# Kernel tuning notes

Measured on AMD Instinct MI355X. Metric: run time of the kernel, lower is better.

The kernel has to match this reference:

```python
import jax, jax.numpy as jnp
import numpy as np

EPS = 1e-12

def l2norm(x, axis):
    # torch.nn.functional.normalize: x / max(||x||_2, eps)
    n = jnp.sqrt(jnp.sum(x * x, axis=axis, keepdims=True))
    return x / jnp.maximum(n, EPS)

def setup_inputs() -> dict:
    key = jax.random.key(0)
    k1, k2, k3, k4 = jax.random.split(key, 4)
    B, Cf, H, W = 128, 1024, 16, 16
    n_att, dv = 312, 300
    img = jax.random.normal(k1, (B, Cf, H, W), dtype=jnp.float32)
    # V is initialized from row-normalized w2v embeddings in the module
    V = l2norm(jax.random.normal(k2, (n_att, dv), dtype=jnp.float32), axis=1)
    W1 = jax.random.normal(k3, (dv, Cf), dtype=jnp.float32)
    W2 = jax.random.normal(k4, (dv, Cf), dtype=jnp.float32)
    return {"img": img, "V": V, "W1": W1, "W2": W2}

def reference(img, V, W1, W2):
    vv = l2norm(V, axis=1)                               # [i, v]
    B, Cf, H, Wd = img.shape
    av = l2norm(img.reshape(B, Cf, H * Wd), axis=1)      # [b, f, r]
    Q = vv @ W1                                          # [i, f]
    A = jnp.einsum('if,bfr->bir', Q, av)                 # attention logits
    A = jax.nn.softmax(A, axis=-1)
    F_p = jnp.einsum('bir,bfr->bif', A, av)              # attended features
    Pred_att = jnp.einsum('if,bif->bi', vv @ W2, F_p)
    return Pred_att
```

## Files before the change

kernel.cpp:

```cpp
#include <hip/hip_runtime.h>
#include <math.h>

#define NB   128
#define CF   1024
#define RR   256
#define NA   312
#define DV   300
#define M2   320
#define MT   640
#define NKC  32

typedef _Float16 half8  __attribute__((ext_vector_type(8)));
typedef float float16v  __attribute__((ext_vector_type(16)));
typedef float float4v   __attribute__((ext_vector_type(4)));

__device__ __forceinline__ void gll16(const void* g, void* l) {
    __builtin_amdgcn_global_load_lds(
        (const __attribute__((address_space(1))) void*)g,
        (__attribute__((address_space(3))) void*)l, 16, 0, 0);
}

__global__ void k_pq(const float* __restrict__ img, float* __restrict__ ssq4,
                     _Float16* __restrict__ avT,
                     const float* __restrict__ V, const float* __restrict__ W1,
                     const float* __restrict__ W2, _Float16* __restrict__ Qb) {
    int lin = blockIdx.x;
    if (lin < 512) {
        int q = lin & 3, b = lin >> 2;
        int t = threadIdx.x;
        int kk8 = t & 3;
        int rq  = t >> 2;
        float ss0 = 0.f, ss1 = 0.f, ss2 = 0.f, ss3 = 0.f;
        int kc0 = q * 8;
        for (int kc = kc0; kc < kc0 + 8; ++kc) {
            const float* src = img + ((size_t)b * CF + kc * 32 + kk8 * 8) * RR + rq * 4;
            float4v v[8];
            #pragma unroll
            for (int j = 0; j < 8; ++j) v[j] = *(const float4v*)(src + (size_t)j * RR);
            #pragma unroll
            for (int j = 0; j < 8; ++j) {
                ss0 += v[j][0] * v[j][0]; ss1 += v[j][1] * v[j][1];
                ss2 += v[j][2] * v[j][2]; ss3 += v[j][3] * v[j][3];
            }
            _Float16* dst = avT + ((size_t)(b * NKC + kc) * RR + rq * 4) * 32 + kk8 * 8;
            #pragma unroll
            for (int s = 0; s < 4; ++s) {
                half8 o;
                #pragma unroll
                for (int j = 0; j < 8; ++j) o[j] = (_Float16)v[j][s];
                *(half8*)(dst + (size_t)s * 32) = o;
            }
        }
        ss0 += __shfl_xor(ss0, 1, 64); ss0 += __shfl_xor(ss0, 2, 64);
        ss1 += __shfl_xor(ss1, 1, 64); ss1 += __shfl_xor(ss1, 2, 64);
        ss2 += __shfl_xor(ss2, 1, 64); ss2 += __shfl_xor(ss2, 2, 64);
        ss3 += __shfl_xor(ss3, 1, 64); ss3 += __shfl_xor(ss3, 2, 64);
        if (kk8 == 0) {
            float4v sv; sv[0] = ss0; sv[1] = ss1; sv[2] = ss2; sv[3] = ss3;
            *(float4v*)(ssq4 + ((size_t)b * 4 + q) * RR + rq * 4) = sv;
        }
    } else {
        int m   = lin - 512;
        int ib  = m % 160;
        int fch = m / 160;
        int t   = threadIdx.x;
        int f   = fch * 256 + t;
        bool isQ2 = ib >= 80;
        int i0l = (ib - (isQ2 ? 80 : 0)) * 4;
        int i0g = (isQ2 ? M2 : 0) + i0l;
        __shared__ float inv4[4];
        float acc[4] = {0, 0, 0, 0};
        bool zero = (i0l >= NA);
        if (!zero) {
            int row = t >> 6, l64 = t & 63;
            float s = 0.f;
            for (int v = l64; v < DV; v += 64) { float x = V[(i0l + row) * DV + v]; s += x * x; }
            #pragma unroll
            for (int o = 32; o; o >>= 1) s += __shfl_xor(s, o, 64);
            if (l64 == 0) inv4[row] = 1.f / fmaxf(sqrtf(s), 1e-12f);
            __syncthreads();
            const float* W = isQ2 ? W2 : W1;
            for (int v = 0; v < DV; v += 4) {
                float w0 = W[(size_t)(v + 0) * CF + f];
                float w1 = W[(size_t)(v + 1) * CF + f];
                float w2 = W[(size_t)(v + 2) * CF + f];
                float w3 = W[(size_t)(v + 3) * CF + f];
                #pragma unroll
                for (int ii = 0; ii < 4; ++ii) {
                    const float* Vr = V + (size_t)(i0l + ii) * DV + v;
                    acc[ii] += Vr[0] * w0 + Vr[1] * w1 + Vr[2] * w2 + Vr[3] * w3;
                }
            }
            #pragma unroll
            for (int ii = 0; ii < 4; ++ii) acc[ii] *= inv4[ii];
        }
        #pragma unroll
        for (int ii = 0; ii < 4; ++ii)
            Qb[((size_t)(f >> 5) * MT + (i0g + ii)) * 32 + (f & 31)] = (_Float16)acc[ii];
    }
}

__launch_bounds__(256, 2)
__global__ void k_gemm(const _Float16* __restrict__ Qb, const _Float16* __restrict__ avT,
                       const float* __restrict__ ssq4, float* __restrict__ out) {
    int lin  = blockIdx.x;
    int xcd  = lin & 7;
    int slot = lin >> 3;
    int bq   = slot / 5;
    int t2   = slot - bq * 5;
    int b    = bq * 8 + xcd;

    int tid = threadIdx.x;
    int lane = tid & 63, w = tid >> 6;
    int nl = lane & 31, kh = lane >> 5;

    __shared__ __align__(16) char smem[49152];
    _Float16* A0 = (_Float16*)smem;
    _Float16* A1 = (_Float16*)(smem + 8192);
    _Float16* B0 = (_Float16*)(smem + 16384);
    _Float16* B1 = (_Float16*)(smem + 32768);
    float* mred = (float*)smem;
    float* mg   = (float*)(smem + 1024);
    float* sred = (float*)(smem + 1280);
    float* dred = (float*)(smem + 2304);

    float16v acc[4][2];
    #pragma unroll
    for (int i = 0; i < 4; ++i)
        #pragma unroll
        for (int j = 0; j < 2; ++j)
            #pragma unroll
            for (int gi = 0; gi < 16; ++gi) acc[i][j][gi] = 0.f;

    int arow  = tid & 127;
    int akb0  = tid >> 7;
    int grow  = (arow < 64) ? (t2 * 64 + arow) : (M2 + t2 * 64 + (arow - 64));
    size_t a_src0 = (size_t)grow * 32 + akb0 * 8;
    const _Float16* bpanel = avT + (size_t)b * NKC * RR * 32;

    #define STAGE(kc_, Ab, Bb) do {                                                  \
        const _Float16* as_ = Qb + (size_t)(kc_) * MT * 32 + a_src0;                 \
        gll16(as_,      (char*)(Ab) + tid * 16);                                     \
        gll16(as_ + 16, (char*)(Ab) + tid * 16 + 4096);                              \
        const _Float16* bs_ = bpanel + (size_t)(kc_) * RR * 32 + (size_t)tid * 32;   \
        gll16(bs_,      (char*)(Bb) + tid * 16);                                     \
        gll16(bs_ + 8,  (char*)(Bb) + tid * 16 + 4096);                              \
        gll16(bs_ + 16, (char*)(Bb) + tid * 16 + 8192);                              \
        gll16(bs_ + 24, (char*)(Bb) + tid * 16 + 12288);                             \
    } while (0)

    #define COMPUTE(Al, Bl) do {                                                     \
        _Pragma("unroll")                                                            \
        for (int ks = 0; ks < 2; ++ks) {                                             \
            int kb = ks * 2 + kh;                                                    \
            half8 b0f = *(const half8*)((Bl) + ((size_t)kb * 256 + w * 64 + nl) * 8);       \
            half8 b1f = *(const half8*)((Bl) + ((size_t)kb * 256 + w * 64 + 32 + nl) * 8);  \
            _Pragma("unroll")                                                        \
            for (int rf = 0; rf < 4; ++rf) {                                         \
                half8 af = *(const half8*)((Al) + ((size_t)kb * 128 + rf * 32 + nl) * 8);   \
                acc[rf][0] = __builtin_amdgcn_mfma_f32_32x32x16_f16(af, b0f, acc[rf][0], 0, 0, 0); \
                acc[rf][1] = __builtin_amdgcn_mfma_f32_32x32x16_f16(af, b1f, acc[rf][1], 0, 0, 0); \
            }                                                                        \
        }                                                                            \
    } while (0)

    STAGE(0, A0, B0);
    STAGE(1, A1, B1);
    asm volatile("s_waitcnt vmcnt(6)" ::: "memory");
    __builtin_amdgcn_s_barrier();
    __builtin_amdgcn_sched_barrier(0);

    #pragma unroll 1
    for (int kc = 0; kc < NKC - 2; kc += 2) {
        COMPUTE(A0, B0);
        __builtin_amdgcn_s_barrier();
        __builtin_amdgcn_sched_barrier(0);
        STAGE(kc + 2, A0, B0);
        asm volatile("s_waitcnt vmcnt(6)" ::: "memory");
        __builtin_amdgcn_s_barrier();
        __builtin_amdgcn_sched_barrier(0);
        COMPUTE(A1, B1);
        __builtin_amdgcn_s_barrier();
        __builtin_amdgcn_sched_barrier(0);
        STAGE(kc + 3, A1, B1);
        asm volatile("s_waitcnt vmcnt(6)" ::: "memory");
        __builtin_amdgcn_s_barrier();
        __builtin_amdgcn_sched_barrier(0);
    }
    COMPUTE(A0, B0);
    asm volatile("s_waitcnt vmcnt(0)" ::: "memory");
    __builtin_amdgcn_s_barrier();
    __builtin_amdgcn_sched_barrier(0);
    COMPUTE(A1, B1);

    #undef STAGE
    #undef COMPUTE

    const float* sq = ssq4 + (size_t)b * 4 * RR;
    int c0 = w * 64 + nl;
    float p0 = sq[c0]      + sq[RR + c0]      + sq[2 * RR + c0]      + sq[3 * RR + c0];
    float p1 = sq[32 + c0] + sq[RR + 32 + c0] + sq[2 * RR + 32 + c0] + sq[3 * RR + 32 + c0];
    float iv0 = 1.f / fmaxf(sqrtf(p0), 1e-12f);
    float iv1 = 1.f / fmaxf(sqrtf(p1), 1e-12f);
    #pragma unroll
    for (int rf = 0; rf < 4; ++rf)
        #pragma unroll
        for (int gi = 0; gi < 16; ++gi) {
            acc[rf][0][gi] *= iv0;
            acc[rf][1][gi] *= iv1;
        }

    float mx[2][16];
    #pragma unroll
    for (int p = 0; p < 2; ++p)
        #pragma unroll
        for (int gi = 0; gi < 16; ++gi)
            mx[p][gi] = fmaxf(acc[p][0][gi], acc[p][1][gi]);
    #pragma unroll
    for (int off = 1; off <= 16; off <<= 1)
        #pragma unroll
        for (int p = 0; p < 2; ++p)
            #pragma unroll
            for (int gi = 0; gi < 16; ++gi)
                mx[p][gi] = fmaxf(mx[p][gi], __shfl_xor(mx[p][gi], off, 64));
    if (nl == 0) {
        #pragma unroll
        for (int p = 0; p < 2; ++p)
            #pragma unroll
            for (int gi = 0; gi < 16; ++gi) {
                int row = (gi & 3) + 8 * (gi >> 2) + 4 * kh;
                mred[(p * 32 + row) * 4 + w] = mx[p][gi];
            }
    }
    __syncthreads();
    if (tid < 64)
        mg[tid] = fmaxf(fmaxf(mred[tid * 4], mred[tid * 4 + 1]),
                        fmaxf(mred[tid * 4 + 2], mred[tid * 4 + 3]));
    __syncthreads();
    float sp[2][16], dp[2][16];
    #pragma unroll
    for (int p = 0; p < 2; ++p)
        #pragma unroll
        for (int gi = 0; gi < 16; ++gi) {
            int row = (gi & 3) + 8 * (gi >> 2) + 4 * kh;
            float m  = mg[p * 32 + row];
            float e0 = __expf(acc[p][0][gi] - m);
            float e1 = __expf(acc[p][1][gi] - m);
            sp[p][gi] = e0 + e1;
            dp[p][gi] = e0 * acc[p + 2][0][gi] + e1 * acc[p + 2][1][gi];
        }
    #pragma unroll
    for (int off = 1; off <= 16; off <<= 1)
        #pragma unroll
        for (int p = 0; p < 2; ++p)
            #pragma unroll
            for (int gi = 0; gi < 16; ++gi) {
                sp[p][gi] += __shfl_xor(sp[p][gi], off, 64);
                dp[p][gi] += __shfl_xor(dp[p][gi], off, 64);
            }
    if (nl == 0) {
        #pragma unroll
        for (int p = 0; p < 2; ++p)
            #pragma unroll
            for (int gi = 0; gi < 16; ++gi) {
                int row = (gi & 3) + 8 * (gi >> 2) + 4 * kh;
                sred[(p * 32 + row) * 4 + w] = sp[p][gi];
                dred[(p * 32 + row) * 4 + w] = dp[p][gi];
            }
    }
    __syncthreads();
    if (tid < 64) {
        float s = sred[tid * 4] + sred[tid * 4 + 1] + sred[tid * 4 + 2] + sred[tid * 4 + 3];
        float d = dred[tid * 4] + dred[tid * 4 + 1] + dred[tid * 4 + 2] + dred[tid * 4 + 3];
        int ig = t2 * 64 + tid;
        if (ig < NA) out[b * NA + ig] = d / s;
    }
}

extern "C" void kernel_launch(void* const* d_in, const int* in_sizes, int n_in,
                              void* d_out, int out_size, void* d_ws, size_t ws_size,
                              hipStream_t stream) {
    const float* img = (const float*)d_in[0];
    const float* V   = (const float*)d_in[1];
    const float* W1  = (const float*)d_in[2];
    const float* W2  = (const float*)d_in[3];
    float* out = (float*)d_out;

    char* ws = (char*)d_ws;
    size_t off = 0;
    float*    ssq4 = (float*)(ws + off);    off += (size_t)NB * 4 * RR * 4;
    _Float16* avT  = (_Float16*)(ws + off); off += (size_t)NB * CF * RR * 2;
    _Float16* Qb   = (_Float16*)(ws + off); off += (size_t)NKC * MT * 32 * 2;

    k_pq<<<dim3(1152), 256, 0, stream>>>(img, ssq4, avT, V, W1, W2, Qb);
    k_gemm<<<dim3(640), 256, 0, stream>>>(Qb, avT, ssq4, out);
}
```

Measured before the change: 277.7 us.

## Split img transpose into per-chunk blocks and widen Q projection per thread

The img normalize/transpose stage now launches one block per (batch, 32-channel chunk) rather than looping over 8 chunks per block. This gives 4096 small blocks for more memory-level parallelism and stores 32 partial sums of squares that the GEMM kernel reduces. The Q-projection blocks now compute 4 features per thread with vector float4 loads of W over all 1024 features, using 160 blocks instead of 640, and emit half4 stores. The GEMM launch bounds are raised to 3 blocks per CU, which may add register pressure, and the epilogue now does 32 loads per column instead of 4.

```diff
diff --git a/kernel.cpp b/kernel.cpp
--- a/kernel.cpp
+++ b/kernel.cpp
@@ -9,8 +9,10 @@
 #define M2   320
 #define MT   640
 #define NKC  32
+#define NQ   160
 
 typedef _Float16 half8  __attribute__((ext_vector_type(8)));
+typedef _Float16 half4  __attribute__((ext_vector_type(4)));
 typedef float float16v  __attribute__((ext_vector_type(16)));
 typedef float float4v   __attribute__((ext_vector_type(4)));
 
@@ -20,36 +22,36 @@
         (__attribute__((address_space(3))) void*)l, 16, 0, 0);
 }
 
-__global__ void k_pq(const float* __restrict__ img, float* __restrict__ ssq4,
+__launch_bounds__(256, 6)
+__global__ void k_pq(const float* __restrict__ img, float* __restrict__ ssq32,
                      _Float16* __restrict__ avT,
                      const float* __restrict__ V, const float* __restrict__ W1,
                      const float* __restrict__ W2, _Float16* __restrict__ Qb) {
     int lin = blockIdx.x;
-    if (lin < 512) {
-        int q = lin & 3, b = lin >> 2;
-        int t = threadIdx.x;
+    int t = threadIdx.x;
+    if (lin >= NQ) {
+        int m  = lin - NQ;
+        int kc = m & 31;
+        int b  = m >> 5;
         int kk8 = t & 3;
         int rq  = t >> 2;
+        const float* src = img + ((size_t)b * CF + kc * 32 + kk8 * 8) * RR + rq * 4;
+        float4v v[8];
+        #pragma unroll
+        for (int j = 0; j < 8; ++j) v[j] = *(const float4v*)(src + (size_t)j * RR);
         float ss0 = 0.f, ss1 = 0.f, ss2 = 0.f, ss3 = 0.f;
-        int kc0 = q * 8;
-        for (int kc = kc0; kc < kc0 + 8; ++kc) {
-            const float* src = img + ((size_t)b * CF + kc * 32 + kk8 * 8) * RR + rq * 4;
-            float4v v[8];
-            #pragma unroll
-            for (int j = 0; j < 8; ++j) v[j] = *(const float4v*)(src + (size_t)j * RR);
-            #pragma unroll
-            for (int j = 0; j < 8; ++j) {
-                ss0 += v[j][0] * v[j][0]; ss1 += v[j][1] * v[j][1];
-                ss2 += v[j][2] * v[j][2]; ss3 += v[j][3] * v[j][3];
-            }
-            _Float16* dst = avT + ((size_t)(b * NKC + kc) * RR + rq * 4) * 32 + kk8 * 8;
-            #pragma unroll
-            for (int s = 0; s < 4; ++s) {
-                half8 o;
-                #pragma unroll
-                for (int j = 0; j < 8; ++j) o[j] = (_Float16)v[j][s];
-                *(half8*)(dst + (size_t)s * 32) = o;
-            }
+        #pragma unroll
+        for (int j = 0; j < 8; ++j) {
+            ss0 += v[j][0] * v[j][0]; ss1 += v[j][1] * v[j][1];
+            ss2 += v[j][2] * v[j][2]; ss3 += v[j][3] * v[j][3];
+        }
+        _Float16* dst = avT + ((size_t)(b * NKC + kc) * RR + rq * 4) * 32 + kk8 * 8;
+        #pragma unroll
+        for (int s = 0; s < 4; ++s) {
+            half8 o;
+            #pragma unroll
+            for (int j = 0; j < 8; ++j) o[j] = (_Float16)v[j][s];
+            *(half8*)(dst + (size_t)s * 32) = o;
         }
         ss0 += __shfl_xor(ss0, 1, 64); ss0 += __shfl_xor(ss0, 2, 64);
         ss1 += __shfl_xor(ss1, 1, 64); ss1 += __shfl_xor(ss1, 2, 64);
@@ -57,21 +59,20 @@
         ss3 += __shfl_xor(ss3, 1, 64); ss3 += __shfl_xor(ss3, 2, 64);
         if (kk8 == 0) {
             float4v sv; sv[0] = ss0; sv[1] = ss1; sv[2] = ss2; sv[3] = ss3;
-            *(float4v*)(ssq4 + ((size_t)b * 4 + q) * RR + rq * 4) = sv;
+            *(float4v*)(ssq32 + ((size_t)b * NKC + kc) * RR + rq * 4) = sv;
         }
     } else {
-        int m   = lin - 512;
-        int ib  = m % 160;
-        int fch = m / 160;
-        int t   = threadIdx.x;
-        int f   = fch * 256 + t;
+        int ib = lin;
         bool isQ2 = ib >= 80;
         int i0l = (ib - (isQ2 ? 80 : 0)) * 4;
         int i0g = (isQ2 ? M2 : 0) + i0l;
         __shared__ float inv4[4];
-        float acc[4] = {0, 0, 0, 0};
-        bool zero = (i0l >= NA);
-        if (!zero) {
+        float acc[4][4];
+        #pragma unroll
+        for (int ii = 0; ii < 4; ++ii)
+            #pragma unroll
+            for (int j = 0; j < 4; ++j) acc[ii][j] = 0.f;
+        if (i0l < NA) {
             int row = t >> 6, l64 = t & 63;
             float s = 0.f;
             for (int v = l64; v < DV; v += 64) { float x = V[(i0l + row) * DV + v]; s += x * x; }
@@ -79,30 +80,39 @@
             for (int o = 32; o; o >>= 1) s += __shfl_xor(s, o, 64);
             if (l64 == 0) inv4[row] = 1.f / fmaxf(sqrtf(s), 1e-12f);
             __syncthreads();
-            const float* W = isQ2 ? W2 : W1;
-            for (int v = 0; v < DV; v += 4) {
-                float w0 = W[(size_t)(v + 0) * CF + f];
-                float w1 = W[(size_t)(v + 1) * CF + f];
-                float w2 = W[(size_t)(v + 2) * CF + f];
-                float w3 = W[(size_t)(v + 3) * CF + f];
+            const float* W  = isQ2 ? W2 : W1;
+            const float* Vb = V + (size_t)i0l * DV;
+            for (int v = 0; v < DV; v += 2) {
+                float4v w0 = *(const float4v*)(W + (size_t)v * CF + t * 4);
+                float4v w1 = *(const float4v*)(W + (size_t)(v + 1) * CF + t * 4);
                 #pragma unroll
                 for (int ii = 0; ii < 4; ++ii) {
-                    const float* Vr = V + (size_t)(i0l + ii) * DV + v;
-                    acc[ii] += Vr[0] * w0 + Vr[1] * w1 + Vr[2] * w2 + Vr[3] * w3;
+                    float a0 = Vb[(size_t)ii * DV + v];
+                    float a1 = Vb[(size_t)ii * DV + v + 1];
+                    #pragma unroll
+                    for (int j = 0; j < 4; ++j) acc[ii][j] += a0 * w0[j] + a1 * w1[j];
                 }
             }
             #pragma unroll
-            for (int ii = 0; ii < 4; ++ii) acc[ii] *= inv4[ii];
-        }
-        #pragma unroll
-        for (int ii = 0; ii < 4; ++ii)
-            Qb[((size_t)(f >> 5) * MT + (i0g + ii)) * 32 + (f & 31)] = (_Float16)acc[ii];
+            for (int ii = 0; ii < 4; ++ii)
+                #pragma unroll
+                for (int j = 0; j < 4; ++j) acc[ii][j] *= inv4[ii];
+        }
+        int fg = t >> 3;
+        int fo = (t & 7) * 4;
+        #pragma unroll
+        for (int ii = 0; ii < 4; ++ii) {
+            half4 h;
+            #pragma unroll
+            for (int j = 0; j < 4; ++j) h[j] = (_Float16)acc[ii][j];
+            *(half4*)&Qb[((size_t)fg * MT + (i0g + ii)) * 32 + fo] = h;
+        }
     }
 }
 
-__launch_bounds__(256, 2)
+__launch_bounds__(256, 3)
 __global__ void k_gemm(const _Float16* __restrict__ Qb, const _Float16* __restrict__ avT,
-                       const float* __restrict__ ssq4, float* __restrict__ out) {
+                       const float* __restrict__ ssq32, float* __restrict__ out) {
     int lin  = blockIdx.x;
     int xcd  = lin & 7;
     int slot = lin >> 3;
@@ -196,10 +206,14 @@
     #undef STAGE
     #undef COMPUTE
 
-    const float* sq = ssq4 + (size_t)b * 4 * RR;
+    const float* sq = ssq32 + (size_t)b * NKC * RR;
     int c0 = w * 64 + nl;
-    float p0 = sq[c0]      + sq[RR + c0]      + sq[2 * RR + c0]      + sq[3 * RR + c0];
-    float p1 = sq[32 + c0] + sq[RR + 32 + c0] + sq[2 * RR + 32 + c0] + sq[3 * RR + 32 + c0];
+    float p0 = 0.f, p1 = 0.f;
+    #pragma unroll
+    for (int kc = 0; kc < NKC; ++kc) {
+        p0 += sq[(size_t)kc * RR + c0];
+        p1 += sq[(size_t)kc * RR + 32 + c0];
+    }
     float iv0 = 1.f / fmaxf(sqrtf(p0), 1e-12f);
     float iv1 = 1.f / fmaxf(sqrtf(p1), 1e-12f);
     #pragma unroll
@@ -288,10 +302,10 @@
 
     char* ws = (char*)d_ws;
     size_t off = 0;
-    float*    ssq4 = (float*)(ws + off);    off += (size_t)NB * 4 * RR * 4;
-    _Float16* avT  = (_Float16*)(ws + off); off += (size_t)NB * CF * RR * 2;
-    _Float16* Qb   = (_Float16*)(ws + off); off += (size_t)NKC * MT * 32 * 2;
-
-    k_pq<<<dim3(1152), 256, 0, stream>>>(img, ssq4, avT, V, W1, W2, Qb);
-    k_gemm<<<dim3(640), 256, 0, stream>>>(Qb, avT, ssq4, out);
+    float*    ssq32 = (float*)(ws + off);    off += (size_t)NB * NKC * RR * 4;
+    _Float16* avT   = (_Float16*)(ws + off); off += (size_t)NB * CF * RR * 2;
+    _Float16* Qb    = (_Float16*)(ws + off); off += (size_t)NKC * MT * 32 * 2;
+
+    k_pq<<<dim3(NQ + NB * NKC), 256, 0, stream>>>(img, ssq32, avT, V, W1, W2, Qb);
+    k_gemm<<<dim3(640), 256, 0, stream>>>(Qb, avT, ssq32, out);
 }
```

After: 307.6 us. 10.8% more time.
